# Optimization experiments

Hardware: AMD Instinct MI355X
Metric: run time of the kernel (lower is better)

The kernel has to match this reference:

```python
import jax, jax.numpy as jnp
import numpy as np

START_IDX = 3
STOP_IDX = 4
NEG = -10000.0
HIDDEN = 1024
K = 5  # tag_set_size
T = 32768


def setup_inputs() -> dict:
    key = jax.random.key(0)
    k1, k2, k3, k4 = jax.random.split(key, 4)
    feats = jax.random.normal(k1, (1, T, HIDDEN), dtype=jnp.float32)
    # hidden2tag Linear params
    W = jax.random.normal(k2, (K, HIDDEN), dtype=jnp.float32) * (1.0 / np.sqrt(HIDDEN))
    b = jax.random.normal(k3, (K,), dtype=jnp.float32) * 0.01
    # transitions ~ Normal(0.5, 0.167), with START row and STOP col masked
    transitions = 0.5 + 0.167 * jax.random.normal(k4, (K, K), dtype=jnp.float32)
    transitions = transitions.at[START_IDX, :].set(NEG).at[:, STOP_IDX].set(NEG)
    return {"feats": feats, "W": W, "b": b, "transitions": transitions}


def _viterbi(emissions, transitions):
    # emissions: [T, K]; transitions[next, prev]
    init = jnp.full((K,), NEG, dtype=emissions.dtype).at[START_IDX].set(0.0)

    def step(vvars, emit):
        ntv = vvars[None, :] + transitions          # [next, prev]
        bp = jnp.argmax(ntv, axis=1)                # best prev tag per next tag
        vvars_new = jnp.max(ntv, axis=1) + emit     # [K]
        return vvars_new, bp

    final, bptrs = jax.lax.scan(step, init, emissions)  # bptrs: [T, K] int
    terminal = final + transitions[STOP_IDX]
    best = jnp.argmax(terminal)
    score = terminal[best]

    def back(tag, bp):
        return bp[tag], tag

    # reverse scan reconstructs the best path (START tag is dropped, matching torch)
    _, path = jax.lax.scan(back, best, bptrs, reverse=True)  # [T]
    return score, path


def reference(feats, W, b, transitions):
    # hidden2tag then squeeze(0): emissions [T, K]
    emissions = jnp.einsum('th,kh->tk', feats[0], W) + b
    score, path = _viterbi(emissions, transitions)
    return score, path
```

## Files before the change

kernel.cpp:

```cpp
#include <hip/hip_runtime.h>

#define T_LEN     32768
#define KTAG      5
#define HID       1024
#define START_TAG 3
#define STOP_TAG  4
#define NEGV      (-10000.0f)
#define CHUNK     64
#define NCHUNK    512
#define NSEG      16
#define SEGLEN    32

__global__ __launch_bounds__(256) void k_emis(const float* __restrict__ feats,
                                              const float* __restrict__ W,
                                              const float* __restrict__ b,
                                              float* __restrict__ emis) {
    int tid  = blockIdx.x * 256 + threadIdx.x;
    int row  = tid >> 6;
    int lane = tid & 63;
    if (row >= T_LEN) return;

    const float4* f4 = (const float4*)feats + row * 256;
    const float4* Wq = (const float4*)W;

    float a0 = 0.f, a1 = 0.f, a2 = 0.f, a3 = 0.f, a4 = 0.f;
#pragma unroll
    for (int j = 0; j < 4; ++j) {
        float4 f  = f4[j * 64 + lane];
        float4 w0 = Wq[0 * 256 + j * 64 + lane];
        float4 w1 = Wq[1 * 256 + j * 64 + lane];
        float4 w2 = Wq[2 * 256 + j * 64 + lane];
        float4 w3 = Wq[3 * 256 + j * 64 + lane];
        float4 w4 = Wq[4 * 256 + j * 64 + lane];
        a0 += f.x * w0.x + f.y * w0.y + f.z * w0.z + f.w * w0.w;
        a1 += f.x * w1.x + f.y * w1.y + f.z * w1.z + f.w * w1.w;
        a2 += f.x * w2.x + f.y * w2.y + f.z * w2.z + f.w * w2.w;
        a3 += f.x * w3.x + f.y * w3.y + f.z * w3.z + f.w * w3.w;
        a4 += f.x * w4.x + f.y * w4.y + f.z * w4.z + f.w * w4.w;
    }
#pragma unroll
    for (int s = 1; s < 64; s <<= 1) {
        a0 += __shfl_xor(a0, s, 64);
        a1 += __shfl_xor(a1, s, 64);
        a2 += __shfl_xor(a2, s, 64);
        a3 += __shfl_xor(a3, s, 64);
        a4 += __shfl_xor(a4, s, 64);
    }
    if (lane < KTAG) {
        float r = (lane == 0) ? a0 : (lane == 1) ? a1 : (lane == 2) ? a2
                                   : (lane == 3) ? a3 : a4;
        emis[row * KTAG + lane] = r + b[lane];
    }
}

__global__ __launch_bounds__(64) void k_chunkmat(const float* __restrict__ emis,
                                                 const float* __restrict__ trans,
                                                 float* __restrict__ P) {
    int c    = blockIdx.x;
    int lane = threadIdx.x;
    if (lane >= 25) return;
    int n = lane / 5, p = lane % 5;

    float tr0 = trans[n * 5 + 0], tr1 = trans[n * 5 + 1], tr2 = trans[n * 5 + 2];
    float tr3 = trans[n * 5 + 3], tr4 = trans[n * 5 + 4];

    int t0 = c * CHUNK;
    float A = trans[n * 5 + p] + emis[t0 * KTAG + n];
    for (int j = 1; j < CHUNK; ++j) {
        float e  = emis[(t0 + j) * KTAG + n];
        float q0 = __shfl(A, 0 * 5 + p, 64);
        float q1 = __shfl(A, 1 * 5 + p, 64);
        float q2 = __shfl(A, 2 * 5 + p, 64);
        float q3 = __shfl(A, 3 * 5 + p, 64);
        float q4 = __shfl(A, 4 * 5 + p, 64);
        float m  = tr0 + q0;
        m = fmaxf(m, tr1 + q1);
        m = fmaxf(m, tr2 + q2);
        m = fmaxf(m, tr3 + q3);
        m = fmaxf(m, tr4 + q4);
        A = m + e;
    }
    P[c * 25 + lane] = A;
}

__global__ __launch_bounds__(1024) void k_scan(const float* __restrict__ P,
                                               const float* __restrict__ trans,
                                               float* __restrict__ vc,
                                               float* __restrict__ score_out,
                                               unsigned int* __restrict__ best_out) {
    __shared__ float Pl[NCHUNK * 25];
    __shared__ float Sl[NSEG * 25];
    __shared__ float vsup[NSEG * 5];

    int tid = threadIdx.x;
    for (int i = tid; i < NCHUNK * 25; i += 1024) Pl[i] = P[i];
    __syncthreads();

    int w = tid >> 6, lane = tid & 63;

    if (lane < 25) {
        int n = lane / 5, p = lane % 5;
        float A = Pl[(w * SEGLEN) * 25 + lane];
        for (int j = 1; j < SEGLEN; ++j) {
            const float* Pn = &Pl[(w * SEGLEN + j) * 25 + n * 5];
            float q0 = __shfl(A, 0 * 5 + p, 64);
            float q1 = __shfl(A, 1 * 5 + p, 64);
            float q2 = __shfl(A, 2 * 5 + p, 64);
            float q3 = __shfl(A, 3 * 5 + p, 64);
            float q4 = __shfl(A, 4 * 5 + p, 64);
            float m  = Pn[0] + q0;
            m = fmaxf(m, Pn[1] + q1);
            m = fmaxf(m, Pn[2] + q2);
            m = fmaxf(m, Pn[3] + q3);
            m = fmaxf(m, Pn[4] + q4);
            A = m;
        }
        Sl[w * 25 + lane] = A;
    }
    __syncthreads();

    if (tid < 5) {
        float v = (tid == START_TAG) ? 0.0f : NEGV;
        for (int s = 0; s < NSEG; ++s) {
            vsup[s * 5 + tid] = v;
            float q0 = __shfl(v, 0, 64);
            float q1 = __shfl(v, 1, 64);
            float q2 = __shfl(v, 2, 64);
            float q3 = __shfl(v, 3, 64);
            float q4 = __shfl(v, 4, 64);
            const float* S = &Sl[s * 25 + tid * 5];
            float m = S[0] + q0;
            m = fmaxf(m, S[1] + q1);
            m = fmaxf(m, S[2] + q2);
            m = fmaxf(m, S[3] + q3);
            m = fmaxf(m, S[4] + q4);
            v = m;
        }
        float term = v + trans[STOP_TAG * 5 + tid];
        float c0 = __shfl(term, 0, 64);
        float c1 = __shfl(term, 1, 64);
        float c2 = __shfl(term, 2, 64);
        float c3 = __shfl(term, 3, 64);
        float c4 = __shfl(term, 4, 64);
        float bv = c0; int bi = 0;
        if (c1 > bv) { bv = c1; bi = 1; }
        if (c2 > bv) { bv = c2; bi = 2; }
        if (c3 > bv) { bv = c3; bi = 3; }
        if (c4 > bv) { bv = c4; bi = 4; }
        if (tid == 0) { score_out[0] = bv; best_out[0] = (unsigned int)bi; }
    }
    __syncthreads();

    if (lane < 5) {
        float v = vsup[w * 5 + lane];
        for (int j = 0; j < SEGLEN; ++j) {
            int c = w * SEGLEN + j;
            vc[c * 5 + lane] = v;
            const float* Pn = &Pl[c * 25 + lane * 5];
            float q0 = __shfl(v, 0, 64);
            float q1 = __shfl(v, 1, 64);
            float q2 = __shfl(v, 2, 64);
            float q3 = __shfl(v, 3, 64);
            float q4 = __shfl(v, 4, 64);
            float m  = Pn[0] + q0;
            m = fmaxf(m, Pn[1] + q1);
            m = fmaxf(m, Pn[2] + q2);
            m = fmaxf(m, Pn[3] + q3);
            m = fmaxf(m, Pn[4] + q4);
            v = m;
        }
    }
}

__global__ __launch_bounds__(64) void k_replay(const float* __restrict__ emis,
                                               const float* __restrict__ trans,
                                               const float* __restrict__ vc,
                                               unsigned short* __restrict__ bp16,
                                               unsigned short* __restrict__ F16) {
    int c    = blockIdx.x;
    int lane = threadIdx.x;
    if (lane >= 5) return;
    int n = lane;

    float tr0 = trans[n * 5 + 0], tr1 = trans[n * 5 + 1], tr2 = trans[n * 5 + 2];
    float tr3 = trans[n * 5 + 3], tr4 = trans[n * 5 + 4];

    float v = vc[c * 5 + n];
    int G = n;
    int t0 = c * CHUNK;
    for (int j = 0; j < CHUNK; ++j) {
        int t = t0 + j;
        float e  = emis[t * KTAG + n];
        float q0 = __shfl(v, 0, 64);
        float q1 = __shfl(v, 1, 64);
        float q2 = __shfl(v, 2, 64);
        float q3 = __shfl(v, 3, 64);
        float q4 = __shfl(v, 4, 64);
        float c0 = tr0 + q0, c1 = tr1 + q1, c2 = tr2 + q2, c3 = tr3 + q3, c4 = tr4 + q4;
        float bv = c0; int bp = 0;
        if (c1 > bv) { bv = c1; bp = 1; }
        if (c2 > bv) { bv = c2; bp = 2; }
        if (c3 > bv) { bv = c3; bp = 3; }
        if (c4 > bv) { bv = c4; bp = 4; }
        v = bv + e;
        G = __shfl(G, bp, 64);
        int b0 = __shfl(bp, 0, 64);
        int b1 = __shfl(bp, 1, 64);
        int b2 = __shfl(bp, 2, 64);
        int b3 = __shfl(bp, 3, 64);
        int b4 = __shfl(bp, 4, 64);
        if (lane == 0)
            bp16[t] = (unsigned short)(b0 | (b1 << 3) | (b2 << 6) | (b3 << 9) | (b4 << 12));
    }
    int g0 = __shfl(G, 0, 64);
    int g1 = __shfl(G, 1, 64);
    int g2 = __shfl(G, 2, 64);
    int g3 = __shfl(G, 3, 64);
    int g4 = __shfl(G, 4, 64);
    if (lane == 0)
        F16[c] = (unsigned short)(g0 | (g1 << 3) | (g2 << 6) | (g3 << 9) | (g4 << 12));
}

__global__ __launch_bounds__(64) void k_back(const unsigned short* __restrict__ F16,
                                             const unsigned int* __restrict__ best_in,
                                             unsigned int* __restrict__ Ec) {
    __shared__ unsigned int sm[NSEG];
    __shared__ unsigned int esup[NSEG];
    int lane = threadIdx.x;

    if (lane < NSEG) {
        unsigned int G = 0u | (1u << 3) | (2u << 6) | (3u << 9) | (4u << 12);
        int base = lane * SEGLEN;
        for (int j = SEGLEN - 1; j >= 0; --j) {
            unsigned int f  = F16[base + j];
            unsigned int Gn = 0;
#pragma unroll
            for (int x = 0; x < 5; ++x) {
                unsigned int gx = (G >> (3 * x)) & 7u;
                unsigned int ex = (f >> (3 * gx)) & 7u;
                Gn |= ex << (3 * x);
            }
            G = Gn;
        }
        sm[lane] = G;
    }
    __syncthreads();
    if (lane == 0) {
        unsigned int E = best_in[0];
        for (int s = NSEG - 1; s >= 0; --s) {
            esup[s] = E;
            E = (sm[s] >> (3 * E)) & 7u;
        }
    }
    __syncthreads();
    if (lane < NSEG) {
        unsigned int E = esup[lane];
        int base = lane * SEGLEN;
        for (int j = SEGLEN - 1; j >= 0; --j) {
            Ec[base + j] = E;
            unsigned int f = F16[base + j];
            E = (f >> (3 * E)) & 7u;
        }
    }
}

__global__ __launch_bounds__(64) void k_path(const unsigned short* __restrict__ bp16,
                                             const unsigned int* __restrict__ Ec,
                                             float* __restrict__ out) {
    int c    = blockIdx.x;
    int lane = threadIdx.x;
    int pk   = (int)bp16[c * 64 + lane];
    unsigned int carry = Ec[c];
    unsigned int mypath = 0;
#pragma unroll
    for (int j = 63; j >= 0; --j) {
        int pkj = __shfl(pk, j, 64);
        if (lane == j) mypath = carry;
        carry = ((unsigned int)pkj >> (3 * carry)) & 7u;
    }
    out[1 + c * 64 + lane] = (float)mypath;
}

extern "C" void kernel_launch(void* const* d_in, const int* in_sizes, int n_in,
                              void* d_out, int out_size, void* d_ws, size_t ws_size,
                              hipStream_t stream) {
    const float* feats = (const float*)d_in[0];
    const float* W     = (const float*)d_in[1];
    const float* b     = (const float*)d_in[2];
    const float* trans = (const float*)d_in[3];
    float* out = (float*)d_out;

    char* ws = (char*)d_ws;
    float*          emis = (float*)(ws + 0);
    float*          P    = (float*)(ws + 655360);
    float*          vc   = (float*)(ws + 706560);
    unsigned short* bp16 = (unsigned short*)(ws + 716800);
    unsigned short* F16  = (unsigned short*)(ws + 782336);
    unsigned int*   Ec   = (unsigned int*)(ws + 783360);
    unsigned int*   best = (unsigned int*)(ws + 785408);

    hipLaunchKernelGGL(k_emis,     dim3(8192), dim3(256),  0, stream, feats, W, b, emis);
    hipLaunchKernelGGL(k_chunkmat, dim3(NCHUNK), dim3(64), 0, stream, emis, trans, P);
    hipLaunchKernelGGL(k_scan,     dim3(1), dim3(1024),    0, stream, P, trans, vc, out, best);
    hipLaunchKernelGGL(k_replay,   dim3(NCHUNK), dim3(64), 0, stream, emis, trans, vc, bp16, F16);
    hipLaunchKernelGGL(k_back,     dim3(1), dim3(64),      0, stream, F16, best, Ec);
    hipLaunchKernelGGL(k_path,     dim3(NCHUNK), dim3(64), 0, stream, bp16, Ec, out);
}
```

Before: 254.8 us.

## Fuse Viterbi chunk, scan, replay, and backtrack stages into one cooperative kernel

Replaces five separate launches (chunk matrices, serial scan, replay, backtrack, path) with one cooperative kernel that uses grid.sync between phases. Emissions and backpointers for each chunk stay in LDS instead of going through global memory. The single-block scan now uses 4 waves with 128-chunk segments instead of 16 waves with 32-chunk segments. This removes per-launch overhead and the bp16 round trip, but adds grid-wide barrier cost and makes the serial scan phase longer per wave.

Measured after the change: 439.5 us. 1.72x slower.

```diff
diff --git a/kernel.cpp b/kernel.cpp
--- a/kernel.cpp
+++ b/kernel.cpp
@@ -1,15 +1,19 @@
 #include <hip/hip_runtime.h>
+#include <hip/hip_cooperative_groups.h>
+
+namespace cg = cooperative_groups;
 
 #define T_LEN     32768
 #define KTAG      5
-#define HID       1024
 #define START_TAG 3
 #define STOP_TAG  4
 #define NEGV      (-10000.0f)
 #define CHUNK     64
 #define NCHUNK    512
-#define NSEG      16
-#define SEGLEN    32
+#define NSEG_S    4
+#define SEGLEN_S  128
+#define NSEG_B    16
+#define SEGLEN_B  32
 
 __global__ __launch_bounds__(256) void k_emis(const float* __restrict__ feats,
                                               const float* __restrict__ W,
@@ -53,232 +57,221 @@
     }
 }
 
-__global__ __launch_bounds__(64) void k_chunkmat(const float* __restrict__ emis,
+__global__ __launch_bounds__(256) void k_viterbi(const float* __restrict__ emis,
                                                  const float* __restrict__ trans,
-                                                 float* __restrict__ P) {
-    int c    = blockIdx.x;
-    int lane = threadIdx.x;
-    if (lane >= 25) return;
-    int n = lane / 5, p = lane % 5;
-
-    float tr0 = trans[n * 5 + 0], tr1 = trans[n * 5 + 1], tr2 = trans[n * 5 + 2];
-    float tr3 = trans[n * 5 + 3], tr4 = trans[n * 5 + 4];
-
-    int t0 = c * CHUNK;
-    float A = trans[n * 5 + p] + emis[t0 * KTAG + n];
-    for (int j = 1; j < CHUNK; ++j) {
-        float e  = emis[(t0 + j) * KTAG + n];
-        float q0 = __shfl(A, 0 * 5 + p, 64);
-        float q1 = __shfl(A, 1 * 5 + p, 64);
-        float q2 = __shfl(A, 2 * 5 + p, 64);
-        float q3 = __shfl(A, 3 * 5 + p, 64);
-        float q4 = __shfl(A, 4 * 5 + p, 64);
-        float m  = tr0 + q0;
-        m = fmaxf(m, tr1 + q1);
-        m = fmaxf(m, tr2 + q2);
-        m = fmaxf(m, tr3 + q3);
-        m = fmaxf(m, tr4 + q4);
-        A = m + e;
-    }
-    P[c * 25 + lane] = A;
-}
-
-__global__ __launch_bounds__(1024) void k_scan(const float* __restrict__ P,
-                                               const float* __restrict__ trans,
-                                               float* __restrict__ vc,
-                                               float* __restrict__ score_out,
-                                               unsigned int* __restrict__ best_out) {
-    __shared__ float Pl[NCHUNK * 25];
-    __shared__ float Sl[NSEG * 25];
-    __shared__ float vsup[NSEG * 5];
-
-    int tid = threadIdx.x;
-    for (int i = tid; i < NCHUNK * 25; i += 1024) Pl[i] = P[i];
+                                                 float* __restrict__ P_g,
+                                                 float* __restrict__ vc_g,
+                                                 unsigned short* __restrict__ F16,
+                                                 unsigned int* __restrict__ Ec,
+                                                 unsigned int* __restrict__ best_g,
+                                                 float* __restrict__ out) {
+    cg::grid_group grid = cg::this_grid();
+
+    __shared__ float          Pl[NCHUNK * 25];
+    __shared__ float          Sl[NSEG_S * 25];
+    __shared__ float          vsup[NSEG_S * 5];
+    __shared__ float          emis_lds[CHUNK * KTAG];
+    __shared__ unsigned short bp_lds[CHUNK];
+    __shared__ unsigned int   sm[NSEG_B];
+    __shared__ unsigned int   esup[NSEG_B];
+
+    int b    = blockIdx.x;
+    int tid  = threadIdx.x;
+    int w    = tid >> 6;
+    int lane = tid & 63;
+
+    for (int i = tid; i < CHUNK * KTAG; i += 256)
+        emis_lds[i] = emis[b * CHUNK * KTAG + i];
     __syncthreads();
 
-    int w = tid >> 6, lane = tid & 63;
-
-    if (lane < 25) {
+    if (w == 0 && lane < 25) {
         int n = lane / 5, p = lane % 5;
-        float A = Pl[(w * SEGLEN) * 25 + lane];
-        for (int j = 1; j < SEGLEN; ++j) {
-            const float* Pn = &Pl[(w * SEGLEN + j) * 25 + n * 5];
+        float tr0 = trans[n * 5 + 0], tr1 = trans[n * 5 + 1], tr2 = trans[n * 5 + 2];
+        float tr3 = trans[n * 5 + 3], tr4 = trans[n * 5 + 4];
+        float A = trans[n * 5 + p] + emis_lds[0 * 5 + n];
+        for (int j = 1; j < CHUNK; ++j) {
+            float e  = emis_lds[j * 5 + n];
             float q0 = __shfl(A, 0 * 5 + p, 64);
             float q1 = __shfl(A, 1 * 5 + p, 64);
             float q2 = __shfl(A, 2 * 5 + p, 64);
             float q3 = __shfl(A, 3 * 5 + p, 64);
             float q4 = __shfl(A, 4 * 5 + p, 64);
-            float m  = Pn[0] + q0;
-            m = fmaxf(m, Pn[1] + q1);
-            m = fmaxf(m, Pn[2] + q2);
-            m = fmaxf(m, Pn[3] + q3);
-            m = fmaxf(m, Pn[4] + q4);
-            A = m;
-        }
-        Sl[w * 25 + lane] = A;
-    }
-    __syncthreads();
-
-    if (tid < 5) {
-        float v = (tid == START_TAG) ? 0.0f : NEGV;
-        for (int s = 0; s < NSEG; ++s) {
-            vsup[s * 5 + tid] = v;
+            float m  = tr0 + q0;
+            m = fmaxf(m, tr1 + q1);
+            m = fmaxf(m, tr2 + q2);
+            m = fmaxf(m, tr3 + q3);
+            m = fmaxf(m, tr4 + q4);
+            A = m + e;
+        }
+        P_g[b * 25 + lane] = A;
+    }
+    grid.sync();
+
+    if (b == 0) {
+        for (int i = tid; i < NCHUNK * 25; i += 256) Pl[i] = P_g[i];
+        __syncthreads();
+        if (lane < 25) {
+            int n = lane / 5, p = lane % 5;
+            float A = Pl[(w * SEGLEN_S) * 25 + lane];
+            for (int j = 1; j < SEGLEN_S; ++j) {
+                const float* Pn = &Pl[(w * SEGLEN_S + j) * 25 + n * 5];
+                float q0 = __shfl(A, 0 * 5 + p, 64);
+                float q1 = __shfl(A, 1 * 5 + p, 64);
+                float q2 = __shfl(A, 2 * 5 + p, 64);
+                float q3 = __shfl(A, 3 * 5 + p, 64);
+                float q4 = __shfl(A, 4 * 5 + p, 64);
+                float m  = Pn[0] + q0;
+                m = fmaxf(m, Pn[1] + q1);
+                m = fmaxf(m, Pn[2] + q2);
+                m = fmaxf(m, Pn[3] + q3);
+                m = fmaxf(m, Pn[4] + q4);
+                A = m;
+            }
+            Sl[w * 25 + lane] = A;
+        }
+        __syncthreads();
+        if (tid < 5) {
+            float v = (tid == START_TAG) ? 0.0f : NEGV;
+            for (int s = 0; s < NSEG_S; ++s) {
+                vsup[s * 5 + tid] = v;
+                float q0 = __shfl(v, 0, 64);
+                float q1 = __shfl(v, 1, 64);
+                float q2 = __shfl(v, 2, 64);
+                float q3 = __shfl(v, 3, 64);
+                float q4 = __shfl(v, 4, 64);
+                const float* S = &Sl[s * 25 + tid * 5];
+                float m = S[0] + q0;
+                m = fmaxf(m, S[1] + q1);
+                m = fmaxf(m, S[2] + q2);
+                m = fmaxf(m, S[3] + q3);
+                m = fmaxf(m, S[4] + q4);
+                v = m;
+            }
+            float term = v + trans[STOP_TAG * 5 + tid];
+            float c0 = __shfl(term, 0, 64);
+            float c1 = __shfl(term, 1, 64);
+            float c2 = __shfl(term, 2, 64);
+            float c3 = __shfl(term, 3, 64);
+            float c4 = __shfl(term, 4, 64);
+            float bv = c0; int bi = 0;
+            if (c1 > bv) { bv = c1; bi = 1; }
+            if (c2 > bv) { bv = c2; bi = 2; }
+            if (c3 > bv) { bv = c3; bi = 3; }
+            if (c4 > bv) { bv = c4; bi = 4; }
+            if (tid == 0) { out[0] = bv; best_g[0] = (unsigned int)bi; }
+        }
+        __syncthreads();
+        if (lane < 5) {
+            float v = vsup[w * 5 + lane];
+            for (int j = 0; j < SEGLEN_S; ++j) {
+                int c = w * SEGLEN_S + j;
+                vc_g[c * 5 + lane] = v;
+                const float* Pn = &Pl[c * 25 + lane * 5];
+                float q0 = __shfl(v, 0, 64);
+                float q1 = __shfl(v, 1, 64);
+                float q2 = __shfl(v, 2, 64);
+                float q3 = __shfl(v, 3, 64);
+                float q4 = __shfl(v, 4, 64);
+                float m  = Pn[0] + q0;
+                m = fmaxf(m, Pn[1] + q1);
+                m = fmaxf(m, Pn[2] + q2);
+                m = fmaxf(m, Pn[3] + q3);
+                m = fmaxf(m, Pn[4] + q4);
+                v = m;
+            }
+        }
+    }
+    grid.sync();
+
+    if (w == 0 && lane < 5) {
+        int n = lane;
+        float tr0 = trans[n * 5 + 0], tr1 = trans[n * 5 + 1], tr2 = trans[n * 5 + 2];
+        float tr3 = trans[n * 5 + 3], tr4 = trans[n * 5 + 4];
+        float v = vc_g[b * 5 + n];
+        int G = n;
+        for (int j = 0; j < CHUNK; ++j) {
+            float e  = emis_lds[j * 5 + n];
             float q0 = __shfl(v, 0, 64);
             float q1 = __shfl(v, 1, 64);
             float q2 = __shfl(v, 2, 64);
             float q3 = __shfl(v, 3, 64);
             float q4 = __shfl(v, 4, 64);
-            const float* S = &Sl[s * 25 + tid * 5];
-            float m = S[0] + q0;
-            m = fmaxf(m, S[1] + q1);
-            m = fmaxf(m, S[2] + q2);
-            m = fmaxf(m, S[3] + q3);
-            m = fmaxf(m, S[4] + q4);
-            v = m;
-        }
-        float term = v + trans[STOP_TAG * 5 + tid];
-        float c0 = __shfl(term, 0, 64);
-        float c1 = __shfl(term, 1, 64);
-        float c2 = __shfl(term, 2, 64);
-        float c3 = __shfl(term, 3, 64);
-        float c4 = __shfl(term, 4, 64);
-        float bv = c0; int bi = 0;
-        if (c1 > bv) { bv = c1; bi = 1; }
-        if (c2 > bv) { bv = c2; bi = 2; }
-        if (c3 > bv) { bv = c3; bi = 3; }
-        if (c4 > bv) { bv = c4; bi = 4; }
-        if (tid == 0) { score_out[0] = bv; best_out[0] = (unsigned int)bi; }
-    }
-    __syncthreads();
-
-    if (lane < 5) {
-        float v = vsup[w * 5 + lane];
-        for (int j = 0; j < SEGLEN; ++j) {
-            int c = w * SEGLEN + j;
-            vc[c * 5 + lane] = v;
-            const float* Pn = &Pl[c * 25 + lane * 5];
-            float q0 = __shfl(v, 0, 64);
-            float q1 = __shfl(v, 1, 64);
-            float q2 = __shfl(v, 2, 64);
-            float q3 = __shfl(v, 3, 64);
-            float q4 = __shfl(v, 4, 64);
-            float m  = Pn[0] + q0;
-            m = fmaxf(m, Pn[1] + q1);
-            m = fmaxf(m, Pn[2] + q2);
-            m = fmaxf(m, Pn[3] + q3);
-            m = fmaxf(m, Pn[4] + q4);
-            v = m;
-        }
-    }
-}
-
-__global__ __launch_bounds__(64) void k_replay(const float* __restrict__ emis,
-                                               const float* __restrict__ trans,
-                                               const float* __restrict__ vc,
-                                               unsigned short* __restrict__ bp16,
-                                               unsigned short* __restrict__ F16) {
-    int c    = blockIdx.x;
-    int lane = threadIdx.x;
-    if (lane >= 5) return;
-    int n = lane;
-
-    float tr0 = trans[n * 5 + 0], tr1 = trans[n * 5 + 1], tr2 = trans[n * 5 + 2];
-    float tr3 = trans[n * 5 + 3], tr4 = trans[n * 5 + 4];
-
-    float v = vc[c * 5 + n];
-    int G = n;
-    int t0 = c * CHUNK;
-    for (int j = 0; j < CHUNK; ++j) {
-        int t = t0 + j;
-        float e  = emis[t * KTAG + n];
-        float q0 = __shfl(v, 0, 64);
-        float q1 = __shfl(v, 1, 64);
-        float q2 = __shfl(v, 2, 64);
-        float q3 = __shfl(v, 3, 64);
-        float q4 = __shfl(v, 4, 64);
-        float c0 = tr0 + q0, c1 = tr1 + q1, c2 = tr2 + q2, c3 = tr3 + q3, c4 = tr4 + q4;
-        float bv = c0; int bp = 0;
-        if (c1 > bv) { bv = c1; bp = 1; }
-        if (c2 > bv) { bv = c2; bp = 2; }
-        if (c3 > bv) { bv = c3; bp = 3; }
-        if (c4 > bv) { bv = c4; bp = 4; }
-        v = bv + e;
-        G = __shfl(G, bp, 64);
-        int b0 = __shfl(bp, 0, 64);
-        int b1 = __shfl(bp, 1, 64);
-        int b2 = __shfl(bp, 2, 64);
-        int b3 = __shfl(bp, 3, 64);
-        int b4 = __shfl(bp, 4, 64);
+            float c0 = tr0 + q0, c1 = tr1 + q1, c2 = tr2 + q2, c3 = tr3 + q3, c4 = tr4 + q4;
+            float bv = c0; int bp = 0;
+            if (c1 > bv) { bv = c1; bp = 1; }
+            if (c2 > bv) { bv = c2; bp = 2; }
+            if (c3 > bv) { bv = c3; bp = 3; }
+            if (c4 > bv) { bv = c4; bp = 4; }
+            v = bv + e;
+            G = __shfl(G, bp, 64);
+            int b0 = __shfl(bp, 0, 64);
+            int b1 = __shfl(bp, 1, 64);
+            int b2 = __shfl(bp, 2, 64);
+            int b3 = __shfl(bp, 3, 64);
+            int b4 = __shfl(bp, 4, 64);
+            if (lane == 0)
+                bp_lds[j] = (unsigned short)(b0 | (b1 << 3) | (b2 << 6) | (b3 << 9) | (b4 << 12));
+        }
+        int g0 = __shfl(G, 0, 64);
+        int g1 = __shfl(G, 1, 64);
+        int g2 = __shfl(G, 2, 64);
+        int g3 = __shfl(G, 3, 64);
+        int g4 = __shfl(G, 4, 64);
         if (lane == 0)
-            bp16[t] = (unsigned short)(b0 | (b1 << 3) | (b2 << 6) | (b3 << 9) | (b4 << 12));
-    }
-    int g0 = __shfl(G, 0, 64);
-    int g1 = __shfl(G, 1, 64);
-    int g2 = __shfl(G, 2, 64);
-    int g3 = __shfl(G, 3, 64);
-    int g4 = __shfl(G, 4, 64);
-    if (lane == 0)
-        F16[c] = (unsigned short)(g0 | (g1 << 3) | (g2 << 6) | (g3 << 9) | (g4 << 12));
-}
-
-__global__ __launch_bounds__(64) void k_back(const unsigned short* __restrict__ F16,
-                                             const unsigned int* __restrict__ best_in,
-                                             unsigned int* __restrict__ Ec) {
-    __shared__ unsigned int sm[NSEG];
-    __shared__ unsigned int esup[NSEG];
-    int lane = threadIdx.x;
-
-    if (lane < NSEG) {
-        unsigned int G = 0u | (1u << 3) | (2u << 6) | (3u << 9) | (4u << 12);
-        int base = lane * SEGLEN;
-        for (int j = SEGLEN - 1; j >= 0; --j) {
-            unsigned int f  = F16[base + j];
-            unsigned int Gn = 0;
+            F16[b] = (unsigned short)(g0 | (g1 << 3) | (g2 << 6) | (g3 << 9) | (g4 << 12));
+    }
+    grid.sync();
+
+    if (b == 0) {
+        if (tid < NSEG_B) {
+            unsigned int G = 0u | (1u << 3) | (2u << 6) | (3u << 9) | (4u << 12);
+            int base = tid * SEGLEN_B;
+            for (int j = SEGLEN_B - 1; j >= 0; --j) {
+                unsigned int f  = F16[base + j];
+                unsigned int Gn = 0;
 #pragma unroll
-            for (int x = 0; x < 5; ++x) {
-                unsigned int gx = (G >> (3 * x)) & 7u;
-                unsigned int ex = (f >> (3 * gx)) & 7u;
-                Gn |= ex << (3 * x);
-            }
-            G = Gn;
-        }
-        sm[lane] = G;
-    }
-    __syncthreads();
-    if (lane == 0) {
-        unsigned int E = best_in[0];
-        for (int s = NSEG - 1; s >= 0; --s) {
-            esup[s] = E;
-            E = (sm[s] >> (3 * E)) & 7u;
-        }
-    }
-    __syncthreads();
-    if (lane < NSEG) {
-        unsigned int E = esup[lane];
-        int base = lane * SEGLEN;
-        for (int j = SEGLEN - 1; j >= 0; --j) {
-            Ec[base + j] = E;
-            unsigned int f = F16[base + j];
-            E = (f >> (3 * E)) & 7u;
-        }
-    }
-}
-
-__global__ __launch_bounds__(64) void k_path(const unsigned short* __restrict__ bp16,
-                                             const unsigned int* __restrict__ Ec,
-                                             float* __restrict__ out) {
-    int c    = blockIdx.x;
-    int lane = threadIdx.x;
-    int pk   = (int)bp16[c * 64 + lane];
-    unsigned int carry = Ec[c];
-    unsigned int mypath = 0;
+                for (int x = 0; x < 5; ++x) {
+                    unsigned int gx = (G >> (3 * x)) & 7u;
+                    unsigned int ex = (f >> (3 * gx)) & 7u;
+                    Gn |= ex << (3 * x);
+                }
+                G = Gn;
+            }
+            sm[tid] = G;
+        }
+        __syncthreads();
+        if (tid == 0) {
+            unsigned int E = best_g[0];
+            for (int s = NSEG_B - 1; s >= 0; --s) {
+                esup[s] = E;
+                E = (sm[s] >> (3 * E)) & 7u;
+            }
+        }
+        __syncthreads();
+        if (tid < NSEG_B) {
+            unsigned int E = esup[tid];
+            int base = tid * SEGLEN_B;
+            for (int j = SEGLEN_B - 1; j >= 0; --j) {
+                Ec[base + j] = E;
+                unsigned int f = F16[base + j];
+                E = (f >> (3 * E)) & 7u;
+            }
+        }
+    }
+    grid.sync();
+
+    if (w == 0) {
+        int pk = (int)bp_lds[lane];
+        unsigned int carry  = Ec[b];
+        unsigned int mypath = 0;
 #pragma unroll
-    for (int j = 63; j >= 0; --j) {
-        int pkj = __shfl(pk, j, 64);
-        if (lane == j) mypath = carry;
-        carry = ((unsigned int)pkj >> (3 * carry)) & 7u;
-    }
-    out[1 + c * 64 + lane] = (float)mypath;
+        for (int j = CHUNK - 1; j >= 0; --j) {
+            int pkj = __shfl(pk, j, 64);
+            if (lane == j) mypath = carry;
+            carry = ((unsigned int)pkj >> (3 * carry)) & 7u;
+        }
+        out[1 + b * CHUNK + lane] = (float)mypath;
+    }
 }
 
 extern "C" void kernel_launch(void* const* d_in, const int* in_sizes, int n_in,
@@ -286,7 +279,7 @@
                               hipStream_t stream) {
     const float* feats = (const float*)d_in[0];
     const float* W     = (const float*)d_in[1];
-    const float* b     = (const float*)d_in[2];
+    const float* bias  = (const float*)d_in[2];
     const float* trans = (const float*)d_in[3];
     float* out = (float*)d_out;
 
@@ -294,15 +287,14 @@
     float*          emis = (float*)(ws + 0);
     float*          P    = (float*)(ws + 655360);
     float*          vc   = (float*)(ws + 706560);
-    unsigned short* bp16 = (unsigned short*)(ws + 716800);
     unsigned short* F16  = (unsigned short*)(ws + 782336);
     unsigned int*   Ec   = (unsigned int*)(ws + 783360);
     unsigned int*   best = (unsigned int*)(ws + 785408);
 
-    hipLaunchKernelGGL(k_emis,     dim3(8192), dim3(256),  0, stream, feats, W, b, emis);
-    hipLaunchKernelGGL(k_chunkmat, dim3(NCHUNK), dim3(64), 0, stream, emis, trans, P);
-    hipLaunchKernelGGL(k_scan,     dim3(1), dim3(1024),    0, stream, P, trans, vc, out, best);
-    hipLaunchKernelGGL(k_replay,   dim3(NCHUNK), dim3(64), 0, stream, emis, trans, vc, bp16, F16);
-    hipLaunchKernelGGL(k_back,     dim3(1), dim3(64),      0, stream, F16, best, Ec);
-    hipLaunchKernelGGL(k_path,     dim3(NCHUNK), dim3(64), 0, stream, bp16, Ec, out);
+    hipLaunchKernelGGL(k_emis, dim3(8192), dim3(256), 0, stream, feats, W, bias, emis);
+
+    void* args[] = { (void*)&emis, (void*)&trans, (void*)&P, (void*)&vc,
+                     (void*)&F16, (void*)&Ec, (void*)&best, (void*)&out };
+    hipLaunchCooperativeKernel((const void*)k_viterbi, dim3(NCHUNK), dim3(256),
+                               args, 0, stream);
 }
```
